# Kernel optimization log

Hardware: AMD Instinct MI355X
Metric: run time of the kernel (lower is better)

Reference implementation:

```python
import jax, jax.numpy as jnp
import numpy as np

B, T, F, H = 2048, 256, 64, 128


def setup_inputs() -> dict:
    key = jax.random.key(0)
    ks = jax.random.split(key, 9)
    s = 0.1  # small init scale for stable recurrence
    return {
        "x": jax.random.normal(ks[0], (B, T, F), dtype=jnp.float32),
        "W_ih": jax.random.normal(ks[1], (4 * H, F), dtype=jnp.float32) * s,
        "W_hh": jax.random.normal(ks[2], (4 * H, H), dtype=jnp.float32) * s,
        "b_ih": jax.random.normal(ks[3], (4 * H,), dtype=jnp.float32) * s,
        "b_hh": jax.random.normal(ks[4], (4 * H,), dtype=jnp.float32) * s,
        "W1": jax.random.normal(ks[5], (32, H), dtype=jnp.float32) * s,
        "b1": jax.random.normal(ks[6], (32,), dtype=jnp.float32) * s,
        "W2": jax.random.normal(ks[7], (1, 32), dtype=jnp.float32) * s,
        "b2": jax.random.normal(ks[8], (1,), dtype=jnp.float32) * s,
    }


def reference(x, W_ih, W_hh, b_ih, b_hh, W1, b1, W2, b2):
    # Single-layer LSTM (PyTorch gate order i, f, g, o), take last hidden state.
    Bsz, Tlen, _ = x.shape
    Hdim = W_hh.shape[1]
    xt = jnp.swapaxes(x, 0, 1)  # [T, B, F]
    bias = b_ih + b_hh  # [4H]

    def step(carry, xb):
        h, c = carry
        gates = xb @ W_ih.T + h @ W_hh.T + bias  # [B, 4H]
        i, f, g, o = jnp.split(gates, 4, axis=-1)
        i = jax.nn.sigmoid(i)
        f = jax.nn.sigmoid(f)
        g = jnp.tanh(g)
        o = jax.nn.sigmoid(o)
        c = f * c + i * g
        h = o * jnp.tanh(c)
        return (h, c), None

    h0 = jnp.zeros((Bsz, Hdim), dtype=x.dtype)
    c0 = jnp.zeros((Bsz, Hdim), dtype=x.dtype)
    (h_last, _), _ = jax.lax.scan(step, (h0, c0), xt)

    # head: Linear(H,32) -> ReLU -> Linear(32,1) -> Sigmoid -> squeeze(-1)
    z = jax.nn.relu(h_last @ W1.T + b1)
    return jax.nn.sigmoid(z @ W2.T + b2)[:, 0]
```

## Files before the change

### kernel.cpp

```cpp
#include <hip/hip_runtime.h>


#define Bsz   2048
#define Tlen  256
#define Fdim  64
#define Hdim  128
#define G4    512
#define KPAD  200
#define BB    8
#define NTHREADS 512

using bf16x8 = __attribute__((ext_vector_type(8))) __bf16;
using f32x4  = __attribute__((ext_vector_type(4))) float;

__device__ __forceinline__ float fast_rcp(float x) {
#if __has_builtin(__builtin_amdgcn_rcpf)
    return __builtin_amdgcn_rcpf(x);
#else
    return 1.0f / x;
#endif
}
__device__ __forceinline__ float fast_exp2(float x) {
#if __has_builtin(__builtin_amdgcn_exp2f)
    return __builtin_amdgcn_exp2f(x);
#else
    return exp2f(x);
#endif
}
__device__ __forceinline__ float fsig(float x) {
    float e = fast_exp2(-1.4426950408889634f * x);
    return fast_rcp(1.0f + e);
}
__device__ __forceinline__ float ftanh(float x) {
    float e = fast_exp2(-2.8853900817779268f * x);
    return (1.0f - e) * fast_rcp(1.0f + e);
}

__global__ __launch_bounds__(NTHREADS, 2)
void lstm_fused(const float* __restrict__ x,
                const float* __restrict__ W_ih,
                const float* __restrict__ W_hh,
                const float* __restrict__ b_ih,
                const float* __restrict__ b_hh,
                const float* __restrict__ W1,
                const float* __restrict__ b1,
                const float* __restrict__ W2,
                const float* __restrict__ b2,
                float* __restrict__ out)
{
    __shared__ __bf16 Alds[16 * KPAD];
    __shared__ float  gatesL[BB * G4];
    __shared__ float  zbuf[BB * 32];

    const int tid  = threadIdx.x;
    const int wave = tid >> 6;
    const int lane = tid & 63;
    const int quad = lane >> 4;
    const int l16  = lane & 15;
    const int n0   = wave * 64;
    const int b0   = blockIdx.x * BB;

    bf16x8 bw[6][4];
    #pragma unroll
    for (int kt = 0; kt < 6; ++kt) {
        const int k0 = kt * 32 + quad * 8;
        #pragma unroll
        for (int nt = 0; nt < 4; ++nt) {
            const int n = n0 + nt * 16 + l16;
            const float* p = (kt < 2) ? (W_ih + n * Fdim + k0)
                                      : (W_hh + n * Hdim + (k0 - Fdim));
            float4 lo = *(const float4*)p;
            float4 hi = *(const float4*)(p + 4);
            bf16x8 r;
            r[0]=(__bf16)lo.x; r[1]=(__bf16)lo.y; r[2]=(__bf16)lo.z; r[3]=(__bf16)lo.w;
            r[4]=(__bf16)hi.x; r[5]=(__bf16)hi.y; r[6]=(__bf16)hi.z; r[7]=(__bf16)hi.w;
            bw[kt][nt] = r;
        }
    }
    float biasv[4];
    #pragma unroll
    for (int nt = 0; nt < 4; ++nt) {
        const int n = n0 + nt * 16 + l16;
        biasv[nt] = b_ih[n] + b_hh[n];
    }

    const int bx = tid >> 6;
    const int fx = tid & 63;
    const float* xp = x + (size_t)(b0 + bx) * (Tlen * Fdim) + fx;

    for (int i = tid; i < 16 * KPAD; i += NTHREADS) Alds[i] = (__bf16)0.0f;
    float x0  = xp[0];
    float xr1 = xp[Fdim];
    __syncthreads();
    Alds[bx * KPAD + fx] = (__bf16)x0;
    __syncthreads();

    float carr[2] = {0.0f, 0.0f};
    const int j_e  = tid & 127;
    const int b_e0 = tid >> 7;

    for (int t = 0; t < Tlen; ++t) {
        float xnext = 0.0f;
        if (t + 2 < Tlen) xnext = xp[(t + 2) * Fdim];

        bf16x8 af[6];
        #pragma unroll
        for (int kt = 0; kt < 6; ++kt)
            af[kt] = *(const bf16x8*)&Alds[l16 * KPAD + kt * 32 + quad * 8];

        #pragma unroll
        for (int nt = 0; nt < 4; ++nt) {
            f32x4 acc = {biasv[nt], biasv[nt], biasv[nt], biasv[nt]};
            #pragma unroll
            for (int kt = 0; kt < 6; ++kt)
                acc = __builtin_amdgcn_mfma_f32_16x16x32_bf16(af[kt], bw[kt][nt], acc, 0, 0, 0);
            if (quad < 2) {
                const int col  = n0 + nt * 16 + l16;
                const int rowb = quad * 4;
                #pragma unroll
                for (int r = 0; r < 4; ++r)
                    gatesL[(rowb + r) * G4 + col] = acc[r];
            }
        }
        __syncthreads();

        #pragma unroll
        for (int it = 0; it < 2; ++it) {
            const int b = b_e0 + 4 * it;
            const float* g = gatesL + b * G4 + j_e;
            float gi = g[0], gf = g[128], gg = g[256], go = g[384];
            float iv = fsig(gi), fv = fsig(gf), gv = ftanh(gg), ov = fsig(go);
            float c = fv * carr[it] + iv * gv;
            carr[it] = c;
            float h = ov * ftanh(c);
            Alds[b * KPAD + Fdim + j_e] = (__bf16)h;
            if (t == Tlen - 1) gatesL[b * G4 + j_e] = h;
        }
        if (t + 1 < Tlen) Alds[bx * KPAD + fx] = (__bf16)xr1;
        xr1 = xnext;
        __syncthreads();
    }

    if (tid < 256) {
        const int b = tid >> 5, n = tid & 31;
        const float4* w4 = (const float4*)(W1 + n * Hdim);
        const float4* h4 = (const float4*)(gatesL + b * G4);
        float s = b1[n];
        #pragma unroll
        for (int kk = 0; kk < Hdim / 4; ++kk) {
            float4 w = w4[kk];
            float4 h = h4[kk];
            s += w.x * h.x + w.y * h.y + w.z * h.z + w.w * h.w;
        }
        zbuf[b * 32 + n] = fmaxf(s, 0.0f);
    }
    __syncthreads();
    if (tid < 8) {
        float s = b2[0];
        #pragma unroll
        for (int n = 0; n < 32; ++n) s += zbuf[tid * 32 + n] * W2[n];
        out[b0 + tid] = fsig(s);
    }
}

extern "C" void kernel_launch(void* const* d_in, const int* in_sizes, int n_in,
                              void* d_out, int out_size, void* d_ws, size_t ws_size,
                              hipStream_t stream) {
    const float* x    = (const float*)d_in[0];
    const float* W_ih = (const float*)d_in[1];
    const float* W_hh = (const float*)d_in[2];
    const float* b_ih = (const float*)d_in[3];
    const float* b_hh = (const float*)d_in[4];
    const float* W1   = (const float*)d_in[5];
    const float* b1   = (const float*)d_in[6];
    const float* W2   = (const float*)d_in[7];
    const float* b2   = (const float*)d_in[8];
    float* out = (float*)d_out;

    dim3 grid(Bsz / BB), block(NTHREADS);
    lstm_fused<<<grid, block, 0, stream>>>(x, W_ih, W_hh, b_ih, b_hh, W1, b1, W2, b2, out);
}
```

Before: 405.4 us.

## Remap gate columns per wave and double-buffer A tile to drop per-step barrier

```diff
diff --git a/kernel.cpp b/kernel.cpp
--- a/kernel.cpp
+++ b/kernel.cpp
@@ -5,10 +5,11 @@
 #define Tlen  256
 #define Fdim  64
 #define Hdim  128
-#define G4    512
-#define KPAD  200
 #define BB    8
 #define NTHREADS 512
+#define TILE_E 512
+#define NKT   6
+#define BUF_E (NKT * TILE_E)
 
 using bf16x8 = __attribute__((ext_vector_type(8))) __bf16;
 using f32x4  = __attribute__((ext_vector_type(4))) float;
@@ -28,8 +29,7 @@
 #endif
 }
 __device__ __forceinline__ float fsig(float x) {
-    float e = fast_exp2(-1.4426950408889634f * x);
-    return fast_rcp(1.0f + e);
+    return fast_rcp(1.0f + fast_exp2(-1.4426950408889634f * x));
 }
 __device__ __forceinline__ float ftanh(float x) {
     float e = fast_exp2(-2.8853900817779268f * x);
@@ -48,109 +48,133 @@
                 const float* __restrict__ b2,
                 float* __restrict__ out)
 {
-    __shared__ __bf16 Alds[16 * KPAD];
-    __shared__ float  gatesL[BB * G4];
+    __shared__ __bf16 Abuf[2][BUF_E];
+    __shared__ float  hlast[BB * Hdim];
     __shared__ float  zbuf[BB * 32];
 
     const int tid  = threadIdx.x;
-    const int wave = tid >> 6;
+    const int w    = tid >> 6;
     const int lane = tid & 63;
     const int quad = lane >> 4;
     const int l16  = lane & 15;
-    const int n0   = wave * 64;
     const int b0   = blockIdx.x * BB;
 
-    bf16x8 bw[6][4];
+    bf16x8 bw[NKT][4];
     #pragma unroll
-    for (int kt = 0; kt < 6; ++kt) {
+    for (int kt = 0; kt < NKT; ++kt) {
         const int k0 = kt * 32 + quad * 8;
         #pragma unroll
-        for (int nt = 0; nt < 4; ++nt) {
-            const int n = n0 + nt * 16 + l16;
-            const float* p = (kt < 2) ? (W_ih + n * Fdim + k0)
-                                      : (W_hh + n * Hdim + (k0 - Fdim));
+        for (int g = 0; g < 4; ++g) {
+            const int n = g * Hdim + w * 16 + l16;
+            const float* p = (kt < 2) ? (W_ih + (size_t)n * Fdim + k0)
+                                      : (W_hh + (size_t)n * Hdim + (k0 - Fdim));
             float4 lo = *(const float4*)p;
             float4 hi = *(const float4*)(p + 4);
             bf16x8 r;
             r[0]=(__bf16)lo.x; r[1]=(__bf16)lo.y; r[2]=(__bf16)lo.z; r[3]=(__bf16)lo.w;
             r[4]=(__bf16)hi.x; r[5]=(__bf16)hi.y; r[6]=(__bf16)hi.z; r[7]=(__bf16)hi.w;
-            bw[kt][nt] = r;
+            bw[kt][g] = r;
         }
     }
     float biasv[4];
     #pragma unroll
-    for (int nt = 0; nt < 4; ++nt) {
-        const int n = n0 + nt * 16 + l16;
-        biasv[nt] = b_ih[n] + b_hh[n];
-    }
-
-    const int bx = tid >> 6;
-    const int fx = tid & 63;
-    const float* xp = x + (size_t)(b0 + bx) * (Tlen * Fdim) + fx;
-
-    for (int i = tid; i < 16 * KPAD; i += NTHREADS) Alds[i] = (__bf16)0.0f;
-    float x0  = xp[0];
-    float xr1 = xp[Fdim];
+    for (int g = 0; g < 4; ++g) {
+        const int n = g * Hdim + w * 16 + l16;
+        biasv[g] = b_ih[n] + b_hh[n];
+    }
+
+    const bool sx_on  = tid < 256;
+    const int  sx_row = tid & 7;
+    const int  sx_fp  = (tid >> 3) & 31;
+    const float* xrp  = x + (size_t)(b0 + sx_row) * (Tlen * Fdim) + 2 * sx_fp;
+    const int sx_elem = (sx_fp >> 4) * TILE_E
+                      + ((((sx_fp >> 2) & 3) * 16 + sx_row) * 8) + 2 * (sx_fp & 3);
+
+    const int er0 = (quad < 2) ? quad * 4 : (quad - 2) * 4 + 2;
+    const int hc  = w * 16 + l16;
+    const int hw_elem = (2 + (hc >> 5)) * TILE_E
+                      + ((((hc >> 3) & 3) * 16 + er0) * 8) + (hc & 7);
+
+    for (int i = tid; i < 2 * BUF_E; i += NTHREADS)
+        ((__bf16*)Abuf)[i] = (__bf16)0.0f;
+    float2 xpre = make_float2(0.f, 0.f);
+    if (sx_on) xpre = *(const float2*)xrp;
     __syncthreads();
-    Alds[bx * KPAD + fx] = (__bf16)x0;
+    if (sx_on) {
+        Abuf[0][sx_elem]     = (__bf16)xpre.x;
+        Abuf[0][sx_elem + 1] = (__bf16)xpre.y;
+        xpre = *(const float2*)(xrp + Fdim);
+    }
     __syncthreads();
 
-    float carr[2] = {0.0f, 0.0f};
-    const int j_e  = tid & 127;
-    const int b_e0 = tid >> 7;
-
+    float cc0 = 0.f, cc1 = 0.f;
+
+    #pragma unroll 2
     for (int t = 0; t < Tlen; ++t) {
-        float xnext = 0.0f;
-        if (t + 2 < Tlen) xnext = xp[(t + 2) * Fdim];
-
-        bf16x8 af[6];
-        #pragma unroll
-        for (int kt = 0; kt < 6; ++kt)
-            af[kt] = *(const bf16x8*)&Alds[l16 * KPAD + kt * 32 + quad * 8];
-
-        #pragma unroll
-        for (int nt = 0; nt < 4; ++nt) {
-            f32x4 acc = {biasv[nt], biasv[nt], biasv[nt], biasv[nt]};
+        const int p = t & 1;
+        const __bf16* rb   = Abuf[p];
+        __bf16*       wbuf = (__bf16*)Abuf[1 - p];
+
+        bf16x8 af[NKT];
+        #pragma unroll
+        for (int kt = 0; kt < NKT; ++kt)
+            af[kt] = *(const bf16x8*)&rb[kt * TILE_E + lane * 8];
+
+        float2 xnext = make_float2(0.f, 0.f);
+        if (sx_on && (t + 2) < Tlen)
+            xnext = *(const float2*)(xrp + (size_t)(t + 2) * Fdim);
+
+        f32x4 acc[4];
+        #pragma unroll
+        for (int g = 0; g < 4; ++g)
+            acc[g] = (f32x4){biasv[g], biasv[g], biasv[g], biasv[g]};
+        #pragma unroll
+        for (int kt = 0; kt < NKT; ++kt) {
             #pragma unroll
-            for (int kt = 0; kt < 6; ++kt)
-                acc = __builtin_amdgcn_mfma_f32_16x16x32_bf16(af[kt], bw[kt][nt], acc, 0, 0, 0);
-            if (quad < 2) {
-                const int col  = n0 + nt * 16 + l16;
-                const int rowb = quad * 4;
-                #pragma unroll
-                for (int r = 0; r < 4; ++r)
-                    gatesL[(rowb + r) * G4 + col] = acc[r];
-            }
-        }
-        __syncthreads();
-
-        #pragma unroll
-        for (int it = 0; it < 2; ++it) {
-            const int b = b_e0 + 4 * it;
-            const float* g = gatesL + b * G4 + j_e;
-            float gi = g[0], gf = g[128], gg = g[256], go = g[384];
-            float iv = fsig(gi), fv = fsig(gf), gv = ftanh(gg), ov = fsig(go);
-            float c = fv * carr[it] + iv * gv;
-            carr[it] = c;
-            float h = ov * ftanh(c);
-            Alds[b * KPAD + Fdim + j_e] = (__bf16)h;
-            if (t == Tlen - 1) gatesL[b * G4 + j_e] = h;
-        }
-        if (t + 1 < Tlen) Alds[bx * KPAD + fx] = (__bf16)xr1;
-        xr1 = xnext;
+            for (int g = 0; g < 4; ++g)
+                acc[g] = __builtin_amdgcn_mfma_f32_16x16x32_bf16(af[kt], bw[kt][g], acc[g], 0, 0, 0);
+        }
+
+        float ga[4][2];
+        #pragma unroll
+        for (int g = 0; g < 4; ++g) {
+            float s2 = __shfl_xor(acc[g][2], 32);
+            float s3 = __shfl_xor(acc[g][3], 32);
+            ga[g][0] = (quad < 2) ? acc[g][0] : s2;
+            ga[g][1] = (quad < 2) ? acc[g][1] : s3;
+        }
+
+        #pragma unroll
+        for (int s = 0; s < 2; ++s) {
+            float iv = fsig(ga[0][s]);
+            float fv = fsig(ga[1][s]);
+            float gv = ftanh(ga[2][s]);
+            float ov = fsig(ga[3][s]);
+            float c  = fv * (s ? cc1 : cc0) + iv * gv;
+            if (s) cc1 = c; else cc0 = c;
+            float h  = ov * ftanh(c);
+            wbuf[hw_elem + 8 * s] = (__bf16)h;
+            if (t == Tlen - 1) hlast[(er0 + s) * Hdim + hc] = h;
+        }
+
+        if (sx_on && (t + 1) < Tlen) {
+            wbuf[sx_elem]     = (__bf16)xpre.x;
+            wbuf[sx_elem + 1] = (__bf16)xpre.y;
+        }
+        xpre = xnext;
         __syncthreads();
     }
 
     if (tid < 256) {
         const int b = tid >> 5, n = tid & 31;
         const float4* w4 = (const float4*)(W1 + n * Hdim);
-        const float4* h4 = (const float4*)(gatesL + b * G4);
+        const float4* h4 = (const float4*)(hlast + b * Hdim);
         float s = b1[n];
         #pragma unroll
         for (int kk = 0; kk < Hdim / 4; ++kk) {
-            float4 w = w4[kk];
-            float4 h = h4[kk];
-            s += w.x * h.x + w.y * h.y + w.z * h.z + w.w * h.w;
+            float4 wv = w4[kk];
+            float4 hv = h4[kk];
+            s += wv.x * hv.x + wv.y * hv.y + wv.z * hv.z + wv.w * hv.w;
         }
         zbuf[b * 32 + n] = fmaxf(s, 0.0f);
     }
```

Result: no change. 409.0 us (+0.9%).

## Transpose LSTM MFMA so gates stay in registers, 16 rows per block

Applied to the files above, without the earlier changes.

```diff
diff --git a/kernel.cpp b/kernel.cpp
--- a/kernel.cpp
+++ b/kernel.cpp
@@ -1,14 +1,11 @@
 #include <hip/hip_runtime.h>
 
 
-#define Bsz   2048
-#define Tlen  256
-#define Fdim  64
-#define Hdim  128
-#define G4    512
-#define KPAD  200
-#define BB    8
-#define NTHREADS 512
+#define Tlen 256
+#define Fdim 64
+#define Hdim 128
+#define ROWS 16
+#define NTH  512
 
 using bf16x8 = __attribute__((ext_vector_type(8))) __bf16;
 using f32x4  = __attribute__((ext_vector_type(4))) float;
@@ -28,15 +25,14 @@
 #endif
 }
 __device__ __forceinline__ float fsig(float x) {
-    float e = fast_exp2(-1.4426950408889634f * x);
-    return fast_rcp(1.0f + e);
+    return fast_rcp(1.0f + fast_exp2(-1.4426950408889634f * x));
 }
 __device__ __forceinline__ float ftanh(float x) {
     float e = fast_exp2(-2.8853900817779268f * x);
     return (1.0f - e) * fast_rcp(1.0f + e);
 }
 
-__global__ __launch_bounds__(NTHREADS, 2)
+__global__ __launch_bounds__(NTH, 2)
 void lstm_fused(const float* __restrict__ x,
                 const float* __restrict__ W_ih,
                 const float* __restrict__ W_hh,
@@ -48,118 +44,174 @@
                 const float* __restrict__ b2,
                 float* __restrict__ out)
 {
-    __shared__ __bf16 Alds[16 * KPAD];
-    __shared__ float  gatesL[BB * G4];
-    __shared__ float  zbuf[BB * 32];
+    __shared__ __bf16 Zh[2][4 * 512];
+    __shared__ __bf16 Xb[2][2 * 512];
+    __shared__ float  hlast[ROWS * Hdim];
+    __shared__ float  zbuf[ROWS * 32];
 
     const int tid  = threadIdx.x;
-    const int wave = tid >> 6;
+    const int w    = tid >> 6;
     const int lane = tid & 63;
     const int quad = lane >> 4;
     const int l16  = lane & 15;
-    const int n0   = wave * 64;
-    const int b0   = blockIdx.x * BB;
-
-    bf16x8 bw[6][4];
+    const int b0   = blockIdx.x * ROWS;
+
+    bf16x8 wf[6][4];
     #pragma unroll
     for (int kt = 0; kt < 6; ++kt) {
         const int k0 = kt * 32 + quad * 8;
         #pragma unroll
-        for (int nt = 0; nt < 4; ++nt) {
-            const int n = n0 + nt * 16 + l16;
-            const float* p = (kt < 2) ? (W_ih + n * Fdim + k0)
-                                      : (W_hh + n * Hdim + (k0 - Fdim));
+        for (int g = 0; g < 4; ++g) {
+            const int m = 128 * g + 16 * w + l16;
+            const float* p = (kt < 2) ? (W_ih + (size_t)m * Fdim + k0)
+                                      : (W_hh + (size_t)m * Hdim + (k0 - 64));
             float4 lo = *(const float4*)p;
             float4 hi = *(const float4*)(p + 4);
             bf16x8 r;
             r[0]=(__bf16)lo.x; r[1]=(__bf16)lo.y; r[2]=(__bf16)lo.z; r[3]=(__bf16)lo.w;
             r[4]=(__bf16)hi.x; r[5]=(__bf16)hi.y; r[6]=(__bf16)hi.z; r[7]=(__bf16)hi.w;
-            bw[kt][nt] = r;
-        }
-    }
-    float biasv[4];
+            wf[kt][g] = r;
+        }
+    }
+    f32x4 bias4[4];
     #pragma unroll
-    for (int nt = 0; nt < 4; ++nt) {
-        const int n = n0 + nt * 16 + l16;
-        biasv[nt] = b_ih[n] + b_hh[n];
-    }
-
-    const int bx = tid >> 6;
-    const int fx = tid & 63;
-    const float* xp = x + (size_t)(b0 + bx) * (Tlen * Fdim) + fx;
-
-    for (int i = tid; i < 16 * KPAD; i += NTHREADS) Alds[i] = (__bf16)0.0f;
-    float x0  = xp[0];
-    float xr1 = xp[Fdim];
-    __syncthreads();
-    Alds[bx * KPAD + fx] = (__bf16)x0;
-    __syncthreads();
-
-    float carr[2] = {0.0f, 0.0f};
-    const int j_e  = tid & 127;
-    const int b_e0 = tid >> 7;
-
-    for (int t = 0; t < Tlen; ++t) {
-        float xnext = 0.0f;
-        if (t + 2 < Tlen) xnext = xp[(t + 2) * Fdim];
-
-        bf16x8 af[6];
-        #pragma unroll
-        for (int kt = 0; kt < 6; ++kt)
-            af[kt] = *(const bf16x8*)&Alds[l16 * KPAD + kt * 32 + quad * 8];
-
-        #pragma unroll
-        for (int nt = 0; nt < 4; ++nt) {
-            f32x4 acc = {biasv[nt], biasv[nt], biasv[nt], biasv[nt]};
+    for (int g = 0; g < 4; ++g)
+        #pragma unroll
+        for (int r = 0; r < 4; ++r) {
+            const int m = 128 * g + 16 * w + quad * 4 + r;
+            bias4[g][r] = b_ih[m] + b_hh[m];
+        }
+
+    const int s  = tid & 15;
+    const int fp = tid >> 4;
+    const float* xrp = x + (size_t)(b0 + s) * (Tlen * Fdim) + 2 * fp;
+    const int x_elem = (fp >> 4) * 512 + ((((fp >> 2) & 3) * 16 + s) * 8) + (fp & 3) * 2;
+
+    const int kt_h   = w >> 1;
+    const int qb_h   = (2 * w + (quad >> 1)) & 3;
+    const int h_elem = kt_h * 512 + (qb_h * 16 + l16) * 8 + (quad & 1) * 4;
+
+    for (int i = tid; i < 2 * 4 * 512; i += NTH) ((__bf16*)Zh)[i] = (__bf16)0.0f;
+    float2 v0 = *(const float2*)xrp;
+    float2 v1 = *(const float2*)(xrp + Fdim);
+    {
+        __bf16 a0[2] = {(__bf16)v0.x, (__bf16)v0.y};
+        __bf16 a1[2] = {(__bf16)v1.x, (__bf16)v1.y};
+        *(uint*)&Xb[0][x_elem] = *(uint*)a0;
+        *(uint*)&Xb[1][x_elem] = *(uint*)a1;
+    }
+    __syncthreads();
+
+    f32x4 xaccA[4], xaccB[4];
+    {
+        bf16x8 x0f[2], x1f[2];
+        #pragma unroll
+        for (int kt = 0; kt < 2; ++kt) {
+            x0f[kt] = *(const bf16x8*)&Xb[0][kt * 512 + lane * 8];
+            x1f[kt] = *(const bf16x8*)&Xb[1][kt * 512 + lane * 8];
+        }
+        #pragma unroll
+        for (int g = 0; g < 4; ++g) { xaccA[g] = bias4[g]; xaccB[g] = bias4[g]; }
+        #pragma unroll
+        for (int kt = 0; kt < 2; ++kt)
             #pragma unroll
-            for (int kt = 0; kt < 6; ++kt)
-                acc = __builtin_amdgcn_mfma_f32_16x16x32_bf16(af[kt], bw[kt][nt], acc, 0, 0, 0);
-            if (quad < 2) {
-                const int col  = n0 + nt * 16 + l16;
-                const int rowb = quad * 4;
-                #pragma unroll
-                for (int r = 0; r < 4; ++r)
-                    gatesL[(rowb + r) * G4 + col] = acc[r];
+            for (int g = 0; g < 4; ++g) {
+                xaccA[g] = __builtin_amdgcn_mfma_f32_16x16x32_bf16(wf[kt][g], x0f[kt], xaccA[g], 0, 0, 0);
+                xaccB[g] = __builtin_amdgcn_mfma_f32_16x16x32_bf16(wf[kt][g], x1f[kt], xaccB[g], 0, 0, 0);
             }
-        }
-        __syncthreads();
-
-        #pragma unroll
-        for (int it = 0; it < 2; ++it) {
-            const int b = b_e0 + 4 * it;
-            const float* g = gatesL + b * G4 + j_e;
-            float gi = g[0], gf = g[128], gg = g[256], go = g[384];
-            float iv = fsig(gi), fv = fsig(gf), gv = ftanh(gg), ov = fsig(go);
-            float c = fv * carr[it] + iv * gv;
-            carr[it] = c;
-            float h = ov * ftanh(c);
-            Alds[b * KPAD + Fdim + j_e] = (__bf16)h;
-            if (t == Tlen - 1) gatesL[b * G4 + j_e] = h;
-        }
-        if (t + 1 < Tlen) Alds[bx * KPAD + fx] = (__bf16)xr1;
-        xr1 = xnext;
-        __syncthreads();
-    }
-
-    if (tid < 256) {
+    }
+    __syncthreads();
+    {
+        float2 v2 = *(const float2*)(xrp + 2 * Fdim);
+        __bf16 a2[2] = {(__bf16)v2.x, (__bf16)v2.y};
+        *(uint*)&Xb[0][x_elem] = *(uint*)a2;
+    }
+    __syncthreads();
+
+    float cst[4] = {0.f, 0.f, 0.f, 0.f};
+    const float* xptr = xrp + 3 * Fdim;
+
+#define STEP(T, P, XACC)                                                        \
+    {                                                                           \
+        const int t = (T);                                                      \
+                                                  \
+        bf16x8 hf[4], xf[2];                                                    \
+        _Pragma("unroll")                                                       \
+        for (int kt = 0; kt < 4; ++kt)                                          \
+            hf[kt] = *(const bf16x8*)&Zh[P][kt * 512 + lane * 8];               \
+        xf[0] = *(const bf16x8*)&Xb[P][lane * 8];                               \
+        xf[1] = *(const bf16x8*)&Xb[P][512 + lane * 8];                         \
+        const bool do_x = (t + 3) < Tlen;                                       \
+        float2 xg = make_float2(0.f, 0.f);                                      \
+        if (do_x) xg = *(const float2*)(xptr + (t - tt) * Fdim);                \
+                                               \
+        f32x4 acc[4];                                                           \
+        _Pragma("unroll")                                                       \
+        for (int g = 0; g < 4; ++g) acc[g] = XACC[g];                           \
+        _Pragma("unroll")                                                       \
+        for (int kt = 0; kt < 4; ++kt)                                          \
+            _Pragma("unroll")                                                   \
+            for (int g = 0; g < 4; ++g)                                         \
+                acc[g] = __builtin_amdgcn_mfma_f32_16x16x32_bf16(               \
+                    wf[2 + kt][g], hf[kt], acc[g], 0, 0, 0);                    \
+                                                  \
+        _Pragma("unroll")                                                       \
+        for (int g = 0; g < 4; ++g) XACC[g] = bias4[g];                         \
+        _Pragma("unroll")                                                       \
+        for (int kt = 0; kt < 2; ++kt)                                          \
+            _Pragma("unroll")                                                   \
+            for (int g = 0; g < 4; ++g)                                         \
+                XACC[g] = __builtin_amdgcn_mfma_f32_16x16x32_bf16(              \
+                    wf[kt][g], xf[kt], XACC[g], 0, 0, 0);                       \
+              \
+        __bf16 hv[4];                                                           \
+        _Pragma("unroll")                                                       \
+        for (int r = 0; r < 4; ++r) {                                           \
+            float iv = fsig(acc[0][r]);                                         \
+            float fv = fsig(acc[1][r]);                                         \
+            float gv = ftanh(acc[2][r]);                                        \
+            float ov = fsig(acc[3][r]);                                         \
+            float c  = fv * cst[r] + iv * gv;                                   \
+            cst[r] = c;                                                         \
+            float h = ov * ftanh(c);                                            \
+            hv[r] = (__bf16)h;                                                  \
+            if (t == Tlen - 1)                                                  \
+                hlast[l16 * Hdim + 16 * w + quad * 4 + r] = h;                  \
+        }                                                                       \
+        *(uint2*)&Zh[(P) ^ 1][h_elem] = *(uint2*)hv;                            \
+        if (do_x) {                                                             \
+            __bf16 xa[2] = {(__bf16)xg.x, (__bf16)xg.y};                        \
+            *(uint*)&Xb[(P) ^ 1][x_elem] = *(uint*)xa;                          \
+        }                                                                       \
+        __syncthreads();                                                        \
+    }
+
+    for (int tt = 0; tt < Tlen; tt += 2) {
+        STEP(tt,     0, xaccA)
+        STEP(tt + 1, 1, xaccB)
+        xptr += 2 * Fdim;
+    }
+#undef STEP
+
+    {
         const int b = tid >> 5, n = tid & 31;
         const float4* w4 = (const float4*)(W1 + n * Hdim);
-        const float4* h4 = (const float4*)(gatesL + b * G4);
-        float s = b1[n];
+        const float4* h4 = (const float4*)(hlast + b * Hdim);
+        float sum = b1[n];
         #pragma unroll
         for (int kk = 0; kk < Hdim / 4; ++kk) {
-            float4 w = w4[kk];
-            float4 h = h4[kk];
-            s += w.x * h.x + w.y * h.y + w.z * h.z + w.w * h.w;
-        }
-        zbuf[b * 32 + n] = fmaxf(s, 0.0f);
-    }
-    __syncthreads();
-    if (tid < 8) {
-        float s = b2[0];
-        #pragma unroll
-        for (int n = 0; n < 32; ++n) s += zbuf[tid * 32 + n] * W2[n];
-        out[b0 + tid] = fsig(s);
+            float4 wv = w4[kk];
+            float4 hv = h4[kk];
+            sum += wv.x * hv.x + wv.y * hv.y + wv.z * hv.z + wv.w * hv.w;
+        }
+        zbuf[b * 32 + n] = fmaxf(sum, 0.0f);
+    }
+    __syncthreads();
+    if (tid < ROWS) {
+        float sum = b2[0];
+        #pragma unroll
+        for (int n = 0; n < 32; ++n) sum += zbuf[tid * 32 + n] * W2[n];
+        out[b0 + tid] = fsig(sum);
     }
 }
 
@@ -177,6 +229,6 @@
     const float* b2   = (const float*)d_in[8];
     float* out = (float*)d_out;
 
-    dim3 grid(Bsz / BB), block(NTHREADS);
+    dim3 grid(2048 / ROWS), block(NTH);
     lstm_fused<<<grid, block, 0, stream>>>(x, W_ih, W_hh, b_ih, b_hh, W1, b1, W2, b2, out);
 }
```

Result: slower. 549.1 us (+35.5%).
